# Performance work log

Measured on AMD Instinct MI355X. Metric: run time of the kernel, lower is better.

The kernel has to match this reference:

```python
import jax, jax.numpy as jnp
import numpy as np

INPUT_SIZE = 512
HIDDEN_SIZE = 1024
OUTPUT_SIZE = 32
BATCH = 256
SEQ = 128


def setup_inputs() -> dict:
    key = jax.random.key(0)
    keys = jax.random.split(key, 20)
    stdv = 1.0 / np.sqrt(HIDDEN_SIZE)
    u = lambda k, shape: jax.random.uniform(k, shape, jnp.float32, -stdv, stdv)
    inp = {
        "inputs": jax.random.normal(keys[0], (BATCH, SEQ, INPUT_SIZE), jnp.float32),
        "w_ii": u(keys[1], (HIDDEN_SIZE, INPUT_SIZE)),
        "w_hi": u(keys[2], (HIDDEN_SIZE, HIDDEN_SIZE)),
        "b_ii": u(keys[3], (HIDDEN_SIZE,)),
        "b_hi": u(keys[4], (HIDDEN_SIZE,)),
        "w_if": u(keys[5], (HIDDEN_SIZE, INPUT_SIZE)),
        "w_hf": u(keys[6], (HIDDEN_SIZE, HIDDEN_SIZE)),
        "b_if": u(keys[7], (HIDDEN_SIZE,)),
        "b_hf": u(keys[8], (HIDDEN_SIZE,)),
        "w_io": u(keys[9], (HIDDEN_SIZE, INPUT_SIZE)),
        "w_ho": u(keys[10], (HIDDEN_SIZE, HIDDEN_SIZE)),
        "b_io": u(keys[11], (HIDDEN_SIZE,)),
        "b_ho": u(keys[12], (HIDDEN_SIZE,)),
        "w_ic": u(keys[13], (HIDDEN_SIZE, INPUT_SIZE)),
        "w_hc": u(keys[14], (HIDDEN_SIZE, HIDDEN_SIZE)),
        "b_ic": u(keys[15], (HIDDEN_SIZE,)),
        "b_hc": u(keys[16], (HIDDEN_SIZE,)),
        "w_fc": u(keys[17], (OUTPUT_SIZE, HIDDEN_SIZE)),
    }
    return inp


def reference(inputs, w_ii, w_hi, b_ii, b_hi, w_if, w_hf, b_if, b_hf,
              w_io, w_ho, b_io, b_ho, w_ic, w_hc, b_ic, b_hc, w_fc):
    # Deterministic eval path (train=False): plain hand-rolled LSTM over time,
    # last hidden -> fc -> log_softmax. Gates computed as in the torch code:
    # sigmoid(W_i* x + b_i* + W_h* h + b_h*), tanh for the cell candidate.
    B, T, I = inputs.shape
    H = w_ii.shape[0]

    def step(carry, x_t):  # x_t: [B, I]
        h, c = carry  # [B, H]
        i_g = jax.nn.sigmoid(x_t @ w_ii.T + b_ii + h @ w_hi.T + b_hi)
        f_g = jax.nn.sigmoid(x_t @ w_if.T + b_if + h @ w_hf.T + b_hf)
        g = jnp.tanh(x_t @ w_ic.T + b_ic + h @ w_hc.T + b_hc)
        o_g = jax.nn.sigmoid(x_t @ w_io.T + b_io + h @ w_ho.T + b_ho)
        c_n = f_g * c + i_g * g
        h_n = o_g * jnp.tanh(c_n)
        return (h_n, c_n), None

    h0 = jnp.zeros((B, H), inputs.dtype)
    c0 = jnp.zeros((B, H), inputs.dtype)
    (h_last, _), _ = jax.lax.scan(step, (h0, c0), jnp.swapaxes(inputs, 0, 1))
    logits = h_last @ w_fc.T  # [B, OUTPUT_SIZE]
    return jax.nn.log_softmax(logits, axis=1)
```

## Files before the change

kernel.cpp:

```cpp
#include <hip/hip_runtime.h>
#include <stdint.h>

#define GAS __attribute__((address_space(1)))
#define LAS __attribute__((address_space(3)))

typedef __bf16 v8bf __attribute__((ext_vector_type(8)));
typedef float v4f __attribute__((ext_vector_type(4)));
typedef unsigned short u16;
typedef unsigned long long u64;

constexpr int kB = 256, kT = 128, kI = 512, kH = 1024, kO = 32;
constexpr int kBlocks = 512, kThreads = 256;
constexpr int KSX = kI / 32;
constexpr int KSH = kH / 32;
constexpr int QX = KSX / 4;
constexpr int QH = KSH / 4;

constexpr size_t OFF_FLG = 0;
constexpr size_t OFF_H   = 8192;
constexpr size_t SZ_H    = (size_t)2 * kB * kH * 2;
constexpr size_t OFF_XT  = OFF_H + SZ_H;
constexpr size_t SZ_XT   = (size_t)kB * kT * kI * 2;
constexpr size_t OFF_WIT = OFF_XT + SZ_XT;
constexpr size_t SZ_WIT  = (size_t)kH * kI * 2;
constexpr size_t OFF_WHT = OFF_WIT + 4 * SZ_WIT;
constexpr size_t SZ_WHT  = (size_t)kH * kH * 2;

struct LstmParams {
  const u16* xt;
  const u16* wit[4];
  const u16* wht[4];
  const float* bi[4];
  const float* bh[4];
  const float* wfc;
  float* out;
  unsigned* flags;
  u16* hbuf;
};

static __device__ __forceinline__ float b2f(u16 v) {
  union { float f; uint32_t i; } u; u.i = ((uint32_t)v) << 16; return u.f;
}
static __device__ __forceinline__ u16 f2b(float f) {
  union { float f; uint32_t i; } u; u.f = f;
  return (u16)((u.i + 0x7fffu + ((u.i >> 16) & 1u)) >> 16);
}
static __device__ __forceinline__ float sigm(float x) { return 1.f / (1.f + __expf(-x)); }
static __device__ __forceinline__ float tanh_f(float x) {
  float e = __expf(2.f * x);
  return 1.f - 2.f / (e + 1.f);
}
static __device__ __forceinline__ void ld16c(const void* g, void* l) {
  __builtin_amdgcn_global_load_lds((const GAS uint32_t*)g, (LAS uint32_t*)l, 16, 0, 0x11);
}

__global__ __launch_bounds__(256) void cvt_x_tile(const float* __restrict__ x,
                                                  u16* __restrict__ xt) {
  const int gid = blockIdx.x * 256 + threadIdx.x;
  const int lane = gid & 63;
  const int ks = (gid >> 6) & 15;
  const int mi = (gid >> 10) & 3;
  const int mt = (gid >> 12) & 3;
  const int t  = gid >> 14;
  const int m = mt * 64 + mi * 16 + (lane & 15);
  const int k = ks * 32 + (lane >> 4) * 8;
  const float4* s = (const float4*)(x + ((size_t)m * kT + t) * kI + k);
  const float4 a = s[0], b = s[1];
  uint4 o = {f2b(a.x) | ((uint32_t)f2b(a.y) << 16), f2b(a.z) | ((uint32_t)f2b(a.w) << 16),
             f2b(b.x) | ((uint32_t)f2b(b.y) << 16), f2b(b.z) | ((uint32_t)f2b(b.w) << 16)};
  *(uint4*)(xt + (size_t)gid * 8) = o;
}

__global__ __launch_bounds__(256) void cvt_w_tile(const float* __restrict__ w,
                                                  u16* __restrict__ wt,
                                                  int K, int lgKS) {
  const int gid = blockIdx.x * 256 + threadIdx.x;
  const int lane = gid & 63;
  const int rest = gid >> 6;
  const int ks = rest & ((1 << lgKS) - 1);
  const int ut2 = rest >> lgKS;
  const int u = ut2 * 16 + (lane & 15);
  const int k = ks * 32 + (lane >> 4) * 8;
  const float4* s = (const float4*)(w + (size_t)u * K + k);
  const float4 a = s[0], b = s[1];
  uint4 o = {f2b(a.x) | ((uint32_t)f2b(a.y) << 16), f2b(a.z) | ((uint32_t)f2b(a.w) << 16),
             f2b(b.x) | ((uint32_t)f2b(b.y) << 16), f2b(b.z) | ((uint32_t)f2b(b.w) << 16)};
  *(uint4*)(wt + (size_t)gid * 8) = o;
}

__global__ __launch_bounds__(kThreads, 2) void lstm_kernel(LstmParams p) {
  __shared__ __align__(16) char smem[66560];
  v4f* Red = (v4f*)smem;
  float* Redf = (float*)smem;
  u16* Hout = (u16*)(smem + 65536);
  u16* shFC = (u16*)smem;

  const int tid = threadIdx.x;
  const int lane = tid & 63;
  const int wv = tid >> 6;
  const int blk = blockIdx.x;
  const int mt8 = blk >> 6;
  const int ut = blk & 63;
  const int mt4 = mt8 >> 1;
  const int mib = (mt8 & 1) * 2;

  const int mloc = lane & 15;
  const int q = lane >> 4;
  const int uglob = ut * 16 + mloc;

  unsigned* gflags = p.flags + mt8 * 256;

  float bias[4];
#pragma unroll
  for (int g = 0; g < 4; ++g) bias[g] = p.bi[g][uglob] + p.bh[g][uglob];

  float creg[2] = {0.f, 0.f};

  v8bf bhh[QH][4];
#pragma unroll
  for (int g = 0; g < 4; ++g)
#pragma unroll
    for (int i = 0; i < QH; ++i)
      bhh[i][g] = *((const v8bf*)p.wht[g] + ((size_t)(ut * KSH + wv * QH + i) * 64 + lane));

  for (int t = 0; t < kT; ++t) {
    v4f acc[2][4];
#pragma unroll
    for (int m = 0; m < 2; ++m)
#pragma unroll
      for (int g = 0; g < 4; ++g) acc[m][g] = (v4f){0.f, 0.f, 0.f, 0.f};

    const v8bf* xf = (const v8bf*)p.xt + ((size_t)(t * 4 + mt4) * 4 * KSX) * 64;
#pragma unroll
    for (int i = 0; i < QX; ++i) {
      v8bf bxl[4];
#pragma unroll
      for (int g = 0; g < 4; ++g)
        bxl[g] = *((const v8bf*)p.wit[g] + ((size_t)(ut * KSX + wv * QX + i) * 64 + lane));
#pragma unroll
      for (int ml = 0; ml < 2; ++ml) {
        const v8bf a = xf[(size_t)((mib + ml) * KSX + wv * QX + i) * 64 + lane];
#pragma unroll
        for (int g = 0; g < 4; ++g)
          acc[ml][g] = __builtin_amdgcn_mfma_f32_16x16x32_bf16(a, bxl[g], acc[ml][g], 0, 0, 0);
      }
    }

    if (t > 0) {
      if (wv == 0) {
        while (true) {
          unsigned v = __hip_atomic_load(&gflags[lane * 4], __ATOMIC_RELAXED,
                                         __HIP_MEMORY_SCOPE_AGENT);
          if (__ballot(v >= (unsigned)t) == ~0ull) break;
          __builtin_amdgcn_s_sleep(1);
        }
      }
      __syncthreads();

      const char* hread = (const char*)(p.hbuf + (size_t)(t & 1) * kB * kH);
      char* myHs = smem + wv * 16384;

#define STAGE_ML(ML)                                                          \
  _Pragma("unroll")                                                           \
  for (int i = 0; i < QH; ++i) {                                              \
    const size_t sl = (size_t)((mt4 * 4 + mib + (ML)) * KSH + wv * QH + i);   \
    ld16c(hread + sl * 1024 + lane * 16, myHs + ((ML) * QH + i) * 1024);      \
  }
#define COMPUTE_ML(ML)                                                        \
  _Pragma("unroll")                                                           \
  for (int i = 0; i < QH; ++i) {                                              \
    const v8bf a = *(const v8bf*)(myHs + ((ML) * QH + i) * 1024 + lane * 16); \
    _Pragma("unroll")                                                         \
    for (int g = 0; g < 4; ++g)                                               \
      acc[(ML)][g] = __builtin_amdgcn_mfma_f32_16x16x32_bf16(                 \
          a, bhh[i][g], acc[(ML)][g], 0, 0, 0);                               \
  }

      STAGE_ML(0) STAGE_ML(1)
      asm volatile("s_waitcnt vmcnt(8)" ::: "memory");
      __builtin_amdgcn_sched_barrier(0);
      COMPUTE_ML(0)
      asm volatile("s_waitcnt vmcnt(0)" ::: "memory");
      __builtin_amdgcn_sched_barrier(0);
      COMPUTE_ML(1)
#undef STAGE_ML
#undef COMPUTE_ML
    }

    __syncthreads();

#pragma unroll
    for (int ml = 0; ml < 2; ++ml)
#pragma unroll
      for (int g = 0; g < 4; ++g)
        Red[(wv * 8 + ml * 4 + g) * 64 + lane] = acc[ml][g];
    __syncthreads();

#pragma unroll
    for (int r = 0; r < 2; ++r) {
      const int lrow = wv * 8 + q * 2 + r;
      const int ml = lrow >> 4;
      const int r16 = lrow & 15;
      const int qp = r16 >> 2;
      const int reg = r16 & 3;
      float gacc[4];
#pragma unroll
      for (int g = 0; g < 4; ++g) {
        float s = 0.f;
#pragma unroll
        for (int kq = 0; kq < 4; ++kq)
          s += Redf[((kq * 8 + ml * 4 + g) * 64 + qp * 16 + mloc) * 4 + reg];
        gacc[g] = s;
      }
      const float iv = sigm(gacc[0] + bias[0]);
      const float fv = sigm(gacc[1] + bias[1]);
      const float gv = tanh_f(gacc[2] + bias[2]);
      const float ov = sigm(gacc[3] + bias[3]);
      creg[r] = fv * creg[r] + iv * gv;
      const float hv = ov * tanh_f(creg[r]);
      Hout[lrow * 16 + mloc] = f2b(hv);
    }
    __syncthreads();

    if (tid < 128) {
      u16* hw = p.hbuf + (size_t)((t + 1) & 1) * kB * kH;
      const int run = tid >> 5;
      const int ml = run >> 1;
      const int hbit = run & 1;
      const int idx = tid & 31;
      const int row16 = idx >> 1;
      const int j0 = (idx & 1) * 4;
      const int hi = (ut & 1) * 2 + hbit;
      const u64 v = *(const u64*)&Hout[(ml * 16 + row16) * 16 + hbit * 8 + j0];
      u64* dst = (u64*)((char*)hw +
                        ((size_t)((mt4 * 4 + mib + ml) * KSH + (ut >> 1)) * 1024) +
                        hi * 256 + row16 * 16 + j0 * 2);
      __hip_atomic_store(dst, v, __ATOMIC_RELAXED, __HIP_MEMORY_SCOPE_AGENT);
    }

    __syncthreads();
    if (tid == 0)
      __hip_atomic_fetch_add(&gflags[ut * 4], 1u, __ATOMIC_RELAXED,
                             __HIP_MEMORY_SCOPE_AGENT);
  }

  if (blk < 32) {
    const int gg8 = blk >> 2;
    if (wv == 0) {
      while (true) {
        unsigned v = __hip_atomic_load(&p.flags[gg8 * 256 + lane * 4], __ATOMIC_RELAXED,
                                       __HIP_MEMORY_SCOPE_AGENT);
        if (__ballot(v >= (unsigned)kT) == ~0ull) break;
        __builtin_amdgcn_s_sleep(1);
      }
    }
    __syncthreads();
    {
      const int gg4 = blk >> 3;
      const int mi = (blk >> 1) & 3;
      const int ks2 = tid >> 3;
      const int ug = (tid >> 1) & 3;
      const int rh = tid & 1;
      u64* hf = (u64*)p.hbuf;
#pragma unroll
      for (int rr = 0; rr < 4; ++rr) {
        const int row_l = rh * 4 + rr;
        const int r16 = (blk & 1) * 8 + row_l;
        const int L = r16 | (ug << 4);
        const size_t fi = ((size_t)((gg4 * 4 + mi) * KSH + ks2) * 64 + L) * 2;
        const u64 a = __hip_atomic_load(hf + fi, __ATOMIC_RELAXED, __HIP_MEMORY_SCOPE_AGENT);
        const u64 b = __hip_atomic_load(hf + fi + 1, __ATOMIC_RELAXED, __HIP_MEMORY_SCOPE_AGENT);
        u64* d = (u64*)&shFC[row_l * kH + ks2 * 32 + ug * 8];
        d[0] = a; d[1] = b;
      }
    }
    __syncthreads();
    const int row = tid >> 5;
    const int col = tid & 31;
    const u16* hr = &shFC[row * kH];
    const float* wr = p.wfc + (size_t)col * kH;
    float s = 0.f;
    for (int k = 0; k < kH; k += 4) {
      const float4 w4 = *(const float4*)(wr + k);
      s += b2f(hr[k]) * w4.x + b2f(hr[k + 1]) * w4.y +
           b2f(hr[k + 2]) * w4.z + b2f(hr[k + 3]) * w4.w;
    }
    float mx = s;
#pragma unroll
    for (int off = 16; off; off >>= 1) mx = fmaxf(mx, __shfl_xor(mx, off, 32));
    const float ex = __expf(s - mx);
    float se = ex;
#pragma unroll
    for (int off = 16; off; off >>= 1) se += __shfl_xor(se, off, 32);
    p.out[(blk * 8 + row) * kO + col] = s - mx - __logf(se);
  }
}

extern "C" void kernel_launch(void* const* d_in, const int* in_sizes, int n_in,
                              void* d_out, int out_size, void* d_ws, size_t ws_size,
                              hipStream_t stream) {
  (void)in_sizes; (void)n_in; (void)out_size; (void)ws_size;
  char* ws = (char*)d_ws;

  u16* xt = (u16*)(ws + OFF_XT);
  u16 *wit[4], *wht[4];
  for (int g = 0; g < 4; ++g) {
    wit[g] = (u16*)(ws + OFF_WIT + (size_t)g * SZ_WIT);
    wht[g] = (u16*)(ws + OFF_WHT + (size_t)g * SZ_WHT);
  }

  const int gsrc[4] = {1, 5, 13, 9};

  hipMemsetAsync(d_ws, 0, 8192, stream);

  cvt_x_tile<<<8192, 256, 0, stream>>>((const float*)d_in[0], xt);
  for (int g = 0; g < 4; ++g) {
    cvt_w_tile<<<256, 256, 0, stream>>>((const float*)d_in[gsrc[g]], wit[g], kI, 4);
    cvt_w_tile<<<512, 256, 0, stream>>>((const float*)d_in[gsrc[g] + 1], wht[g], kH, 5);
  }

  LstmParams p;
  p.xt = xt;
  for (int g = 0; g < 4; ++g) {
    p.wit[g] = wit[g];
    p.wht[g] = wht[g];
    p.bi[g] = (const float*)d_in[gsrc[g] + 2];
    p.bh[g] = (const float*)d_in[gsrc[g] + 3];
  }
  p.wfc = (const float*)d_in[17];
  p.out = (float*)d_out;
  p.flags = (unsigned*)(ws + OFF_FLG);
  p.hbuf = (u16*)(ws + OFF_H);

  void* args[] = {&p};
  hipError_t e = hipLaunchCooperativeKernel((void*)lstm_kernel, dim3(kBlocks),
                                            dim3(kThreads), args, 0, stream);
  if (e != hipSuccess) {
    (void)hipGetLastError();
    lstm_kernel<<<dim3(kBlocks), dim3(kThreads), 0, stream>>>(p);
  }
}
```

Measured before the change: 1.216 ms.

## Split persistent LSTM grid to one 16-row batch tile per block

Doubles the persistent grid to 1024 blocks so each block handles a single 16-row batch tile instead of two. Shared memory per block is halved and launch bounds raised to four blocks per CU. Flag groups shrink to 64 blocks each, with the flag stride halved. This spreads the per-step recurrent work across more blocks to cut per-step latency, at the cost of redundant weight register residency, more synchronization participants and more flag traffic.

```diff
diff --git a/kernel.cpp b/kernel.cpp
--- a/kernel.cpp
+++ b/kernel.cpp
@@ -10,7 +10,7 @@
 typedef unsigned long long u64;
 
 constexpr int kB = 256, kT = 128, kI = 512, kH = 1024, kO = 32;
-constexpr int kBlocks = 512, kThreads = 256;
+constexpr int kBlocks = 1024, kThreads = 256;
 constexpr int KSX = kI / 32;
 constexpr int KSH = kH / 32;
 constexpr int QX = KSX / 4;
@@ -88,33 +88,33 @@
   *(uint4*)(wt + (size_t)gid * 8) = o;
 }
 
-__global__ __launch_bounds__(kThreads, 2) void lstm_kernel(LstmParams p) {
-  __shared__ __align__(16) char smem[66560];
+__global__ __launch_bounds__(kThreads, 4) void lstm_kernel(LstmParams p) {
+  __shared__ __align__(16) char smem[33280];
   v4f* Red = (v4f*)smem;
   float* Redf = (float*)smem;
-  u16* Hout = (u16*)(smem + 65536);
+  u16* Hout = (u16*)(smem + 32768);
   u16* shFC = (u16*)smem;
 
   const int tid = threadIdx.x;
   const int lane = tid & 63;
   const int wv = tid >> 6;
   const int blk = blockIdx.x;
-  const int mt8 = blk >> 6;
+  const int mt16 = blk >> 6;
   const int ut = blk & 63;
-  const int mt4 = mt8 >> 1;
-  const int mib = (mt8 & 1) * 2;
+  const int mt4 = mt16 >> 2;
+  const int mi = mt16 & 3;
 
   const int mloc = lane & 15;
   const int q = lane >> 4;
   const int uglob = ut * 16 + mloc;
 
-  unsigned* gflags = p.flags + mt8 * 256;
+  unsigned* gflags = p.flags + mt16 * 128;
 
   float bias[4];
 #pragma unroll
   for (int g = 0; g < 4; ++g) bias[g] = p.bi[g][uglob] + p.bh[g][uglob];
 
-  float creg[2] = {0.f, 0.f};
+  float creg = 0.f;
 
   v8bf bhh[QH][4];
 #pragma unroll
@@ -124,11 +124,9 @@
       bhh[i][g] = *((const v8bf*)p.wht[g] + ((size_t)(ut * KSH + wv * QH + i) * 64 + lane));
 
   for (int t = 0; t < kT; ++t) {
-    v4f acc[2][4];
-#pragma unroll
-    for (int m = 0; m < 2; ++m)
-#pragma unroll
-      for (int g = 0; g < 4; ++g) acc[m][g] = (v4f){0.f, 0.f, 0.f, 0.f};
+    v4f acc[4];
+#pragma unroll
+    for (int g = 0; g < 4; ++g) acc[g] = (v4f){0.f, 0.f, 0.f, 0.f};
 
     const v8bf* xf = (const v8bf*)p.xt + ((size_t)(t * 4 + mt4) * 4 * KSX) * 64;
 #pragma unroll
@@ -137,19 +135,16 @@
 #pragma unroll
       for (int g = 0; g < 4; ++g)
         bxl[g] = *((const v8bf*)p.wit[g] + ((size_t)(ut * KSX + wv * QX + i) * 64 + lane));
-#pragma unroll
-      for (int ml = 0; ml < 2; ++ml) {
-        const v8bf a = xf[(size_t)((mib + ml) * KSX + wv * QX + i) * 64 + lane];
-#pragma unroll
-        for (int g = 0; g < 4; ++g)
-          acc[ml][g] = __builtin_amdgcn_mfma_f32_16x16x32_bf16(a, bxl[g], acc[ml][g], 0, 0, 0);
-      }
+      const v8bf a = xf[(size_t)(mi * KSX + wv * QX + i) * 64 + lane];
+#pragma unroll
+      for (int g = 0; g < 4; ++g)
+        acc[g] = __builtin_amdgcn_mfma_f32_16x16x32_bf16(a, bxl[g], acc[g], 0, 0, 0);
     }
 
     if (t > 0) {
       if (wv == 0) {
         while (true) {
-          unsigned v = __hip_atomic_load(&gflags[lane * 4], __ATOMIC_RELAXED,
+          unsigned v = __hip_atomic_load(&gflags[lane * 2], __ATOMIC_RELAXED,
                                          __HIP_MEMORY_SCOPE_AGENT);
           if (__ballot(v >= (unsigned)t) == ~0ull) break;
           __builtin_amdgcn_s_sleep(1);
@@ -158,97 +153,89 @@
       __syncthreads();
 
       const char* hread = (const char*)(p.hbuf + (size_t)(t & 1) * kB * kH);
-      char* myHs = smem + wv * 16384;
-
-#define STAGE_ML(ML)                                                          \
-  _Pragma("unroll")                                                           \
-  for (int i = 0; i < QH; ++i) {                                              \
-    const size_t sl = (size_t)((mt4 * 4 + mib + (ML)) * KSH + wv * QH + i);   \
-    ld16c(hread + sl * 1024 + lane * 16, myHs + ((ML) * QH + i) * 1024);      \
-  }
-#define COMPUTE_ML(ML)                                                        \
-  _Pragma("unroll")                                                           \
-  for (int i = 0; i < QH; ++i) {                                              \
-    const v8bf a = *(const v8bf*)(myHs + ((ML) * QH + i) * 1024 + lane * 16); \
-    _Pragma("unroll")                                                         \
-    for (int g = 0; g < 4; ++g)                                               \
-      acc[(ML)][g] = __builtin_amdgcn_mfma_f32_16x16x32_bf16(                 \
-          a, bhh[i][g], acc[(ML)][g], 0, 0, 0);                               \
-  }
-
-      STAGE_ML(0) STAGE_ML(1)
-      asm volatile("s_waitcnt vmcnt(8)" ::: "memory");
+      char* myHs = smem + wv * 8192;
+
+#pragma unroll
+      for (int i = 0; i < QH; ++i) {
+        const size_t sl = (size_t)((mt4 * 4 + mi) * KSH + wv * QH + i);
+        ld16c(hread + sl * 1024 + lane * 16, myHs + i * 1024);
+      }
+
+      asm volatile("s_waitcnt vmcnt(4)" ::: "memory");
       __builtin_amdgcn_sched_barrier(0);
-      COMPUTE_ML(0)
+#pragma unroll
+      for (int i = 0; i < 4; ++i) {
+        const v8bf a = *(const v8bf*)(myHs + i * 1024 + lane * 16);
+#pragma unroll
+        for (int g = 0; g < 4; ++g)
+          acc[g] = __builtin_amdgcn_mfma_f32_16x16x32_bf16(a, bhh[i][g], acc[g], 0, 0, 0);
+      }
       asm volatile("s_waitcnt vmcnt(0)" ::: "memory");
       __builtin_amdgcn_sched_barrier(0);
-      COMPUTE_ML(1)
-#undef STAGE_ML
-#undef COMPUTE_ML
-    }
-
-    __syncthreads();
-
-#pragma unroll
-    for (int ml = 0; ml < 2; ++ml)
-#pragma unroll
-      for (int g = 0; g < 4; ++g)
-        Red[(wv * 8 + ml * 4 + g) * 64 + lane] = acc[ml][g];
-    __syncthreads();
-
-#pragma unroll
-    for (int r = 0; r < 2; ++r) {
-      const int lrow = wv * 8 + q * 2 + r;
-      const int ml = lrow >> 4;
-      const int r16 = lrow & 15;
-      const int qp = r16 >> 2;
-      const int reg = r16 & 3;
+#pragma unroll
+      for (int i = 4; i < QH; ++i) {
+        const v8bf a = *(const v8bf*)(myHs + i * 1024 + lane * 16);
+#pragma unroll
+        for (int g = 0; g < 4; ++g)
+          acc[g] = __builtin_amdgcn_mfma_f32_16x16x32_bf16(a, bhh[i][g], acc[g], 0, 0, 0);
+      }
+    }
+
+    __syncthreads();
+
+#pragma unroll
+    for (int g = 0; g < 4; ++g)
+      Red[(wv * 4 + g) * 64 + lane] = acc[g];
+    __syncthreads();
+
+    {
+      const int lrow = wv * 4 + q;
+      const int lanep = (lrow >> 2) * 16 + mloc;
+      const int reg = lrow & 3;
       float gacc[4];
 #pragma unroll
       for (int g = 0; g < 4; ++g) {
         float s = 0.f;
 #pragma unroll
         for (int kq = 0; kq < 4; ++kq)
-          s += Redf[((kq * 8 + ml * 4 + g) * 64 + qp * 16 + mloc) * 4 + reg];
+          s += Redf[((kq * 4 + g) * 64 + lanep) * 4 + reg];
         gacc[g] = s;
       }
       const float iv = sigm(gacc[0] + bias[0]);
       const float fv = sigm(gacc[1] + bias[1]);
       const float gv = tanh_f(gacc[2] + bias[2]);
       const float ov = sigm(gacc[3] + bias[3]);
-      creg[r] = fv * creg[r] + iv * gv;
-      const float hv = ov * tanh_f(creg[r]);
+      creg = fv * creg + iv * gv;
+      const float hv = ov * tanh_f(creg);
       Hout[lrow * 16 + mloc] = f2b(hv);
     }
     __syncthreads();
 
-    if (tid < 128) {
+    if (tid < 64) {
       u16* hw = p.hbuf + (size_t)((t + 1) & 1) * kB * kH;
-      const int run = tid >> 5;
-      const int ml = run >> 1;
-      const int hbit = run & 1;
+      const int hbit = tid >> 5;
       const int idx = tid & 31;
       const int row16 = idx >> 1;
       const int j0 = (idx & 1) * 4;
       const int hi = (ut & 1) * 2 + hbit;
-      const u64 v = *(const u64*)&Hout[(ml * 16 + row16) * 16 + hbit * 8 + j0];
+      const u64 v = *(const u64*)&Hout[row16 * 16 + hbit * 8 + j0];
       u64* dst = (u64*)((char*)hw +
-                        ((size_t)((mt4 * 4 + mib + ml) * KSH + (ut >> 1)) * 1024) +
+                        ((size_t)((mt4 * 4 + mi) * KSH + (ut >> 1)) * 1024) +
                         hi * 256 + row16 * 16 + j0 * 2);
       __hip_atomic_store(dst, v, __ATOMIC_RELAXED, __HIP_MEMORY_SCOPE_AGENT);
     }
 
     __syncthreads();
     if (tid == 0)
-      __hip_atomic_fetch_add(&gflags[ut * 4], 1u, __ATOMIC_RELAXED,
+      __hip_atomic_fetch_add(&gflags[ut * 2], 1u, __ATOMIC_RELAXED,
                              __HIP_MEMORY_SCOPE_AGENT);
   }
 
   if (blk < 32) {
-    const int gg8 = blk >> 2;
+    const int gg16 = blk >> 1;
     if (wv == 0) {
       while (true) {
-        unsigned v = __hip_atomic_load(&p.flags[gg8 * 256 + lane * 4], __ATOMIC_RELAXED,
+        unsigned v = __hip_atomic_load(&p.flags[gg16 * 128 + lane * 2], __ATOMIC_RELAXED,
                                        __HIP_MEMORY_SCOPE_AGENT);
         if (__ballot(v >= (unsigned)kT) == ~0ull) break;
         __builtin_amdgcn_s_sleep(1);
@@ -257,7 +244,7 @@
     __syncthreads();
     {
       const int gg4 = blk >> 3;
-      const int mi = (blk >> 1) & 3;
+      const int fmi = (blk >> 1) & 3;
       const int ks2 = tid >> 3;
       const int ug = (tid >> 1) & 3;
       const int rh = tid & 1;
@@ -267,7 +254,7 @@
         const int row_l = rh * 4 + rr;
         const int r16 = (blk & 1) * 8 + row_l;
         const int L = r16 | (ug << 4);
-        const size_t fi = ((size_t)((gg4 * 4 + mi) * KSH + ks2) * 64 + L) * 2;
+        const size_t fi = ((size_t)((gg4 * 4 + fmi) * KSH + ks2) * 64 + L) * 2;
         const u64 a = __hip_atomic_load(hf + fi, __ATOMIC_RELAXED, __HIP_MEMORY_SCOPE_AGENT);
         const u64 b = __hip_atomic_load(hf + fi + 1, __ATOMIC_RELAXED, __HIP_MEMORY_SCOPE_AGENT);
         u64* d = (u64*)&shFC[row_l * kH + ks2 * 32 + ug * 8];
```

New measurement: 2.194 ms. +80.4%, slower.
